# Optimization experiments

Measured on AMD Instinct MI355X. Metric: run time of the kernel, lower is better.

Reference implementation:

```python
import jax, jax.numpy as jnp
import numpy as np

N, E, Z, H = 16384, 131072, 128, 8
ZH = Z // H
CUTOFF = 5.0


def _dense(key, din, dout, bias=True):
    kw, kb = jax.random.split(key)
    W = (jax.random.normal(kw, (din, dout), jnp.float32) / np.sqrt(din)).astype(jnp.float32)
    if bias:
        return W, jnp.zeros((dout,), jnp.float32)
    return W


def setup_inputs() -> dict:
    key = jax.random.key(0)
    ks = jax.random.split(key, 24)
    edge_index = jax.random.randint(ks[0], (2, E), 0, N)
    h_N_1_Z = jax.random.normal(ks[1], (N, 1, Z), jnp.float32)
    mu_N_L2_Z = jax.random.normal(ks[2], (N, 3, Z), jnp.float32) * 0.1
    ev = jax.random.normal(ks[3], (E, 3), jnp.float32)
    edge_vec_E_3 = ev / jnp.linalg.norm(ev, axis=-1, keepdims=True)
    edge_emb_E_Z = jax.random.normal(ks[4], (E, Z), jnp.float32)
    edge_weight_E = jax.random.uniform(ks[5], (E,), jnp.float32, 0.5, CUTOFF)
    deg = jax.ops.segment_sum(jnp.ones((E,), jnp.float32), edge_index[1], num_segments=N)
    num_edges_expanded_E = deg[edge_index[1]]
    inp = dict(edge_index=edge_index, h_N_1_Z=h_N_1_Z, mu_N_L2_Z=mu_N_L2_Z,
               edge_vec_E_3=edge_vec_E_3, edge_emb_E_Z=edge_emb_E_Z,
               edge_weight_E=edge_weight_E, num_edges_expanded_E=num_edges_expanded_E)
    inp['W_q'], inp['b_q'] = _dense(ks[6], Z, Z)
    inp['W_k'], inp['b_k'] = _dense(ks[7], Z, Z)
    inp['W_gs1'], inp['b_gs1'] = _dense(ks[8], Z, Z)
    inp['W_gs2'], inp['b_gs2'] = _dense(ks[9], Z, 3 * Z)
    inp['W_gv1'], inp['b_gv1'] = _dense(ks[10], Z, Z)
    inp['W_gv2'], inp['b_gv2'] = _dense(ks[11], Z, 3 * Z)
    inp['W_phik'], inp['b_phik'] = _dense(ks[12], Z, Z)
    inp['W_re'], inp['b_re'] = _dense(ks[13], Z, 3 * Z)
    inp['W_vq'] = _dense(ks[14], Z, Z, bias=False)   # vecq_w, no bias
    inp['W_vk0'] = _dense(ks[15], Z, Z, bias=False)  # veck_w[0] (lmax=1), no bias
    inp['W_lin'], inp['b_lin'] = _dense(ks[16], Z, Z)  # lin_w_linear
    inp['W_eu1'], inp['b_eu1'] = _dense(ks[17], Z, Z)  # edge_attr_up MLP [Z,Z,Z]
    inp['W_eu2'], inp['b_eu2'] = _dense(ks[18], Z, Z)
    return inp


def reference(edge_index, h_N_1_Z, mu_N_L2_Z, edge_vec_E_3, edge_emb_E_Z,
              edge_weight_E, num_edges_expanded_E,
              W_q, b_q, W_k, b_k, W_gs1, b_gs1, W_gs2, b_gs2,
              W_gv1, b_gv1, W_gv2, b_gv2, W_phik, b_phik, W_re, b_re,
              W_vq, W_vk0, W_lin, b_lin, W_eu1, b_eu1, W_eu2, b_eu2):
    silu = jax.nn.silu
    src, dst = edge_index[0], edge_index[1]  # messages j->i aggregated at dst=i
    hs = h_N_1_Z[:, 0]                        # (N, Z); layernorm='' -> identity
    q = (hs @ W_q + b_q).reshape(N, H, ZH)
    k = (hs @ W_k + b_k).reshape(N, H, ZH)
    x3 = silu(hs @ W_gs1 + b_gs1) @ W_gs2 + b_gs2    # gamma_s: (N, 3Z)
    val3 = silu(hs @ W_gv1 + b_gv1) @ W_gv2 + b_gv2  # gamma_v: (N, 3Z)
    r_attn = silu(edge_emb_E_Z @ W_phik + b_phik).reshape(E, H, ZH)
    r_ij = edge_emb_E_Z @ W_re + b_re                # (E, 3Z)

    # per-edge multi-head attention with segment softmax over target node
    logits = jnp.sum(q[dst] * k[src] * r_attn, axis=-1)        # (E, H)
    m = jax.ops.segment_max(logits, dst, num_segments=N)
    ex = jnp.exp(logits - m[dst])
    den = jax.ops.segment_sum(ex, dst, num_segments=N)
    attn = ex / den[dst]
    attn = attn * (jnp.sqrt(num_edges_expanded_E)[:, None] / np.float32(np.sqrt(Z)))

    sea = (attn[..., None] * val3[src].reshape(E, H, 3 * ZH)).reshape(E, 3 * Z)
    cut = 0.5 * (jnp.cos(jnp.pi * edge_weight_E / CUTOFF) + 1.0) * (edge_weight_E < CUTOFF)
    x_ij = cut[:, None] * sea * (x3[src] * r_ij)               # (E, 3Z)
    o_s, o_d, o_t = x_ij[:, :Z], x_ij[:, Z:2 * Z], x_ij[:, 2 * Z:]
    dmu_ij = o_d[:, None, :] * edge_vec_E_3[..., None] + o_t[:, None, :] * mu_N_L2_Z[src]  # (E,3,Z)

    h_out = h_N_1_Z + jax.ops.segment_sum(o_s, dst, num_segments=N)[:, None, :]
    mu_out = mu_N_L2_Z + jax.ops.segment_sum(dmu_ij, dst, num_segments=N)

    # edge update (sep_vecj, lmax=1 -> single degree block)
    w1 = jnp.einsum('nlz,ze->nle', mu_out, W_vq)
    w2 = jnp.einsum('nlz,ze->nle', mu_out, W_vk0)
    w1_d = jnp.sum(w1[dst] * edge_vec_E_3[..., None], axis=1)  # (E, evec)
    w2_d = jnp.sum(w2[src] * edge_vec_E_3[..., None], axis=1)
    w_dot = jnp.tanh((w1_d * w2_d) @ W_lin + b_lin)            # gated='gatedt'
    f_up = silu(edge_emb_E_Z @ W_eu1 + b_eu1) @ W_eu2 + b_eu2  # edge_attr_up MLP
    df_ij = edge_emb_E_Z + f_up * w_dot
    return h_out, mu_out, df_ij
```

## Files before the change

### kernel.cpp

```cpp
#include <hip/hip_runtime.h>
#include <math.h>

#define NN 16384
#define EE 131072
#define ZZ 128
#define HH 8

typedef short bf16x8 __attribute__((ext_vector_type(8)));
typedef float f32x4 __attribute__((ext_vector_type(4)));
typedef unsigned short ushort4v __attribute__((ext_vector_type(4)));
typedef unsigned short ushort8v __attribute__((ext_vector_type(8)));

__device__ __forceinline__ float silu_f(float x) { return x / (1.0f + __expf(-x)); }

__device__ __forceinline__ unsigned short f2bf(float x) {
    unsigned u = __float_as_uint(x);
    unsigned r = (u >> 16) & 1u;
    u += 0x7fffu + r;
    return (unsigned short)(u >> 16);
}
__device__ __forceinline__ float bf2f(unsigned short x) {
    return __uint_as_float(((unsigned)x) << 16);
}

__device__ __forceinline__ f32x4 mfma16(bf16x8 a, bf16x8 b, f32x4 c) {
    return __builtin_amdgcn_mfma_f32_16x16x32_bf16(a, b, c, 0, 0, 0);
}

__device__ __forceinline__ unsigned fenc(float x) {
    unsigned b = __float_as_uint(x);
    return (b & 0x80000000u) ? ~b : (b | 0x80000000u);
}
__device__ __forceinline__ float fdec(unsigned e) {
    unsigned b = (e & 0x80000000u) ? (e & 0x7FFFFFFFu) : ~e;
    return __uint_as_float(b);
}

__device__ __forceinline__ void stageB(const unsigned short* Wt, char* lB, int t) {
    const uint4* Wg = (const uint4*)Wt;
#pragma unroll
    for (int i = 0; i < 8; ++i) {
        const int cid = t + i * 256;
        const int n = cid >> 4, c16 = cid & 15;
        *(uint4*)(lB + ((n * 256 + c16 * 16) ^ ((n & 7) << 4))) = Wg[cid];
    }
}

struct WPrep {
    const float* w[13];
    int P[13];
    int tile0[14];
};

__global__ __launch_bounds__(128) void prep_weights(WPrep wp, unsigned short* wt) {
    int b = blockIdx.x, wi = 0;
    while (b >= wp.tile0[wi + 1]) ++wi;
    const int cg = (b - wp.tile0[wi]) * 128;
    const float* w = wp.w[wi];
    unsigned short* o = wt + (size_t)wp.tile0[wi] * 16384;
    const int P = wp.P[wi];
    const int t = threadIdx.x;
    for (int k0 = 0; k0 < 128; k0 += 8) {
        ushort8v v;
#pragma unroll
        for (int j = 0; j < 8; ++j) v[j] = f2bf(w[(size_t)(k0 + j) * P + cg + t]);
        *(ushort8v*)(o + (size_t)(cg + t) * 128 + k0) = v;
    }
}

struct BPrep {
    const float* b[13];
    int off[14];
};

__global__ __launch_bounds__(256) void prep_bias(BPrep bp, float* bcat) {
    const int idx = blockIdx.x * 256 + threadIdx.x;
    if (idx >= 2432) return;
    int wi = 0;
    while (idx >= bp.off[wi + 1]) ++wi;
    bcat[idx] = bp.b[wi] ? bp.b[wi][idx - bp.off[wi]] : 0.f;
}

template <int ACT, int INBF, int DUMP>
__global__ __launch_bounds__(256, 2) void mm_bf16(
    const void* __restrict__ Av, const unsigned short* __restrict__ Wt,
    const float* __restrict__ bias, unsigned short* __restrict__ C,
    const unsigned short* __restrict__ aux, unsigned short* __restrict__ dumpA,
    int P, int As)
{
    __shared__ uint4 lA4[2048];
    __shared__ uint4 lB4[2048];
    char* lA = (char*)lA4;
    char* lB = (char*)lB4;
    const int t = threadIdx.x;
    const size_t row0 = (size_t)blockIdx.x * 128;
    const int cg = blockIdx.y * 128;
    if (INBF) {
        const uint4* Ag = (const uint4*)((const unsigned short*)Av + row0 * As);
        const int rs = As >> 3;
#pragma unroll
        for (int i = 0; i < 8; ++i) {
            const int chunk = t + i * 256;
            const int r = chunk >> 4, c16 = chunk & 15;
            *(uint4*)(lA + ((r * 256 + c16 * 16) ^ ((r & 7) << 4))) = Ag[r * rs + c16];
        }
    } else {
        const float4* Ag = (const float4*)((const float*)Av + row0 * As);
        const int rs = As >> 2;
#pragma unroll
        for (int i = 0; i < 16; ++i) {
            const int f4 = t + i * 256;
            const int r = f4 >> 5, c4 = f4 & 31;
            const float4 v = Ag[r * rs + c4];
            ushort4v bb;
            bb.x = f2bf(v.x); bb.y = f2bf(v.y); bb.z = f2bf(v.z); bb.w = f2bf(v.w);
            *(ushort4v*)(lA + ((r * 256 + c4 * 8) ^ ((r & 7) << 4))) = bb;
        }
    }
    stageB(Wt + (size_t)cg * 128, lB, t);
    __syncthreads();
    if (DUMP) {
#pragma unroll
        for (int i = 0; i < 8; ++i) {
            const int ch = t + i * 256;
            const int row = ch >> 4, cpos = ch & 15;
            const uint4 v = *(const uint4*)(lA + ((row * 256 + cpos * 16) ^ ((row & 7) << 4)));
            *(uint4*)(dumpA + (row0 + row) * 128 + cpos * 8) = v;
        }
    }
    const int lane = t & 63, wid = t >> 6;
    const int rbase = (wid >> 1) * 64, cbase = (wid & 1) * 64;
    const int lr = lane & 15, lgp = lane >> 4;
    f32x4 acc[4][4];
#pragma unroll
    for (int i = 0; i < 4; ++i)
#pragma unroll
        for (int j = 0; j < 4; ++j) acc[i][j] = (f32x4){0.f, 0.f, 0.f, 0.f};
#pragma unroll
    for (int ks = 0; ks < 4; ++ks) {
        bf16x8 av[4], bv[4];
#pragma unroll
        for (int mt = 0; mt < 4; ++mt) {
            const int r = rbase + mt * 16 + lr;
            av[mt] = *(const bf16x8*)(lA + ((r * 256 + ks * 64 + lgp * 16) ^ ((r & 7) << 4)));
        }
#pragma unroll
        for (int nt = 0; nt < 4; ++nt) {
            const int c = cbase + nt * 16 + lr;
            bv[nt] = *(const bf16x8*)(lB + ((c * 256 + ks * 64 + lgp * 16) ^ ((c & 7) << 4)));
        }
#pragma unroll
        for (int mt = 0; mt < 4; ++mt)
#pragma unroll
            for (int nt = 0; nt < 4; ++nt)
                acc[mt][nt] = mfma16(av[mt], bv[nt], acc[mt][nt]);
    }
    __syncthreads();
#pragma unroll
    for (int nt = 0; nt < 4; ++nt) {
        const int col = cbase + nt * 16 + lr;
        const int gcol = cg + col;
        const float b = bias[gcol];
#pragma unroll
        for (int mt = 0; mt < 4; ++mt) {
#pragma unroll
            for (int j = 0; j < 4; ++j) {
                const int row = rbase + mt * 16 + lgp * 4 + j;
                float v = acc[mt][nt][j] + b;
                if (ACT == 1) v = silu_f(v);
                if (ACT == 2) v = v * bf2f(aux[(row0 + row) * (size_t)P + gcol]);
                *(unsigned short*)(lB + ((row * 256 + col * 2) ^ ((row & 7) << 4))) = f2bf(v);
            }
        }
    }
    __syncthreads();
#pragma unroll
    for (int i = 0; i < 8; ++i) {
        const int ch = t + i * 256;
        const int row = ch >> 4, cpos = ch & 15;
        const uint4 v = *(const uint4*)(lB + ((row * 256 + cpos * 16) ^ ((row & 7) << 4)));
        *(uint4*)(C + (row0 + row) * (size_t)P + cg + cpos * 8) = v;
    }
}

__global__ __launch_bounds__(256, 2) void combine_mfma(
    const unsigned short* __restrict__ embb, const unsigned short* __restrict__ Wt_re,
    const float* __restrict__ bre, const float* __restrict__ lg,
    const float* __restrict__ den, const float* __restrict__ nee,
    const int* __restrict__ dst, const float* __restrict__ ew,
    unsigned short* __restrict__ osb, unsigned short* __restrict__ odb,
    unsigned short* __restrict__ otb)
{
    __shared__ uint4 lA4[2048];
    __shared__ uint4 lB4[2048];
    __shared__ float attnS[128 * 8];
    __shared__ float cutS[128];
    char* lA = (char*)lA4;
    char* lB = (char*)lB4;
    const int t = threadIdx.x;
    const size_t e0 = (size_t)blockIdx.x * 128;
    {
        const uint4* Ag = (const uint4*)(embb + e0 * 128);
#pragma unroll
        for (int i = 0; i < 8; ++i) {
            const int chunk = t + i * 256;
            const int r = chunk >> 4, c16 = chunk & 15;
            *(uint4*)(lA + ((r * 256 + c16 * 16) ^ ((r & 7) << 4))) = Ag[chunk];
        }
    }
    stageB(Wt_re, lB, t);
    {
        const int er = t >> 1;
        const size_t e = e0 + er;
        const int h0 = (t & 1) * 4;
        const int d = dst[e];
        const float sc = sqrtf(nee[e]) * 0.08838834764831845f;
        const float4 ex4 = *(const float4*)(lg + e * 8 + h0);
        const float4 dn4 = *(const float4*)(den + (size_t)d * 8 + h0);
        float4 a4;
        a4.x = ex4.x / dn4.x * sc; a4.y = ex4.y / dn4.y * sc;
        a4.z = ex4.z / dn4.z * sc; a4.w = ex4.w / dn4.w * sc;
        *(float4*)(attnS + er * 8 + h0) = a4;
        if ((t & 1) == 0) {
            const float w = ew[e];
            cutS[er] = (w < 5.0f) ? 0.5f * (cosf(w * 0.62831853071795864f) + 1.0f) : 0.0f;
        }
    }
    __syncthreads();
    const int lane = t & 63, wid = t >> 6;
    const int rbase = (wid >> 1) * 64, cbase = (wid & 1) * 64;
    const int lr = lane & 15, lgp = lane >> 4;
    bf16x8 avh[4][4];
#pragma unroll
    for (int ks = 0; ks < 4; ++ks)
#pragma unroll
        for (int mt = 0; mt < 4; ++mt) {
            const int r = rbase + mt * 16 + lr;
            avh[ks][mt] = *(const bf16x8*)(lA + ((r * 256 + ks * 64 + lgp * 16) ^ ((r & 7) << 4)));
        }
    __syncthreads();
    unsigned short* bufs[3] = {osb, odb, otb};
    for (int cg3 = 0; cg3 < 3; ++cg3) {
        f32x4 acc[4][4];
#pragma unroll
        for (int i = 0; i < 4; ++i)
#pragma unroll
            for (int j = 0; j < 4; ++j) acc[i][j] = (f32x4){0.f, 0.f, 0.f, 0.f};
#pragma unroll
        for (int ks = 0; ks < 4; ++ks) {
            bf16x8 bv[4];
#pragma unroll
            for (int nt = 0; nt < 4; ++nt) {
                const int c = cbase + nt * 16 + lr;
                bv[nt] = *(const bf16x8*)(lB + ((c * 256 + ks * 64 + lgp * 16) ^ ((c & 7) << 4)));
            }
#pragma unroll
            for (int mt = 0; mt < 4; ++mt)
#pragma unroll
                for (int nt = 0; nt < 4; ++nt)
                    acc[mt][nt] = mfma16(avh[ks][mt], bv[nt], acc[mt][nt]);
        }
        const int cgo = cg3 * 128;
#pragma unroll
        for (int nt = 0; nt < 4; ++nt) {
            const int col = cbase + nt * 16 + lr;
            const int gcol = cgo + col;
            const int head = gcol / 48;
            const float b = bre[gcol];
#pragma unroll
            for (int mt = 0; mt < 4; ++mt) {
#pragma unroll
                for (int j = 0; j < 4; ++j) {
                    const int row = rbase + mt * 16 + lgp * 4 + j;
                    const float o = (acc[mt][nt][j] + b) * attnS[row * 8 + head] * cutS[row];
                    *(unsigned short*)(lA + ((row * 256 + col * 2) ^ ((row & 7) << 4))) = f2bf(o);
                }
            }
        }
        __syncthreads();
        unsigned short* buf = bufs[cg3];
#pragma unroll
        for (int i = 0; i < 8; ++i) {
            const int ch = t + i * 256;
            const int row = ch >> 4, cpos = ch & 15;
            const uint4 v = *(const uint4*)(lA + ((row * 256 + cpos * 16) ^ ((row & 7) << 4)));
            *(uint4*)(buf + (e0 + row) * 128 + cpos * 8) = v;
        }
        if (cg3 < 2) stageB(Wt_re + (size_t)(cg3 + 1) * 16384, lB, t);
        __syncthreads();
    }
}

__global__ __launch_bounds__(256, 2) void wdot_fused(
    const unsigned short* __restrict__ w12, const float* __restrict__ ev,
    const int* __restrict__ src, const int* __restrict__ dst,
    const unsigned short* __restrict__ Wt_lin, const float* __restrict__ bl,
    const unsigned short* __restrict__ embb, const unsigned short* __restrict__ fup,
    float* __restrict__ df)
{
    __shared__ uint4 lA4[2048];
    __shared__ uint4 lB4[2048];
    char* lA = (char*)lA4;
    char* lB = (char*)lB4;
    const int t = threadIdx.x;
    const size_t e0 = (size_t)blockIdx.x * 128;
    stageB(Wt_lin, lB, t);
#pragma unroll
    for (int i = 0; i < 8; ++i) {
        const int chunk = t + i * 256;
        const int r = chunk >> 4, c8 = chunk & 15;
        const size_t e = e0 + r;
        const int s = src[e], d = dst[e];
        const float e0v = ev[e * 3 + 0], e1v = ev[e * 3 + 1], e2v = ev[e * 3 + 2];
        const ushort8v a0 = *(const ushort8v*)(w12 + ((size_t)d * 3 + 0) * 256 + c8 * 8);
        const ushort8v a1 = *(const ushort8v*)(w12 + ((size_t)d * 3 + 1) * 256 + c8 * 8);
        const ushort8v a2 = *(const ushort8v*)(w12 + ((size_t)d * 3 + 2) * 256 + c8 * 8);
        const ushort8v c0 = *(const ushort8v*)(w12 + ((size_t)s * 3 + 0) * 256 + 128 + c8 * 8);
        const ushort8v c1 = *(const ushort8v*)(w12 + ((size_t)s * 3 + 1) * 256 + 128 + c8 * 8);
        const ushort8v c2 = *(const ushort8v*)(w12 + ((size_t)s * 3 + 2) * 256 + 128 + c8 * 8);
        ushort8v o;
#pragma unroll
        for (int j = 0; j < 8; ++j) {
            const float av = e0v * bf2f(a0[j]) + e1v * bf2f(a1[j]) + e2v * bf2f(a2[j]);
            const float bv = e0v * bf2f(c0[j]) + e1v * bf2f(c1[j]) + e2v * bf2f(c2[j]);
            o[j] = f2bf(av * bv);
        }
        *(ushort8v*)(lA + ((r * 256 + c8 * 16) ^ ((r & 7) << 4))) = o;
    }
    __syncthreads();
    const int lane = t & 63, wid = t >> 6;
    const int rbase = (wid >> 1) * 64, cbase = (wid & 1) * 64;
    const int lr = lane & 15, lgp = lane >> 4;
    f32x4 acc[4][4];
#pragma unroll
    for (int i = 0; i < 4; ++i)
#pragma unroll
        for (int j = 0; j < 4; ++j) acc[i][j] = (f32x4){0.f, 0.f, 0.f, 0.f};
#pragma unroll
    for (int ks = 0; ks < 4; ++ks) {
        bf16x8 av[4], bv[4];
#pragma unroll
        for (int mt = 0; mt < 4; ++mt) {
            const int r = rbase + mt * 16 + lr;
            av[mt] = *(const bf16x8*)(lA + ((r * 256 + ks * 64 + lgp * 16) ^ ((r & 7) << 4)));
        }
#pragma unroll
        for (int nt = 0; nt < 4; ++nt) {
            const int c = cbase + nt * 16 + lr;
            bv[nt] = *(const bf16x8*)(lB + ((c * 256 + ks * 64 + lgp * 16) ^ ((c & 7) << 4)));
        }
#pragma unroll
        for (int mt = 0; mt < 4; ++mt)
#pragma unroll
            for (int nt = 0; nt < 4; ++nt)
                acc[mt][nt] = mfma16(av[mt], bv[nt], acc[mt][nt]);
    }
#pragma unroll
    for (int nt = 0; nt < 4; ++nt) {
        const int col = cbase + nt * 16 + lr;
        const float b = bl[col];
#pragma unroll
        for (int mt = 0; mt < 4; ++mt) {
#pragma unroll
            for (int j = 0; j < 4; ++j) {
                const size_t base = (e0 + rbase + mt * 16 + lgp * 4 + j) * 128 + col;
                const float v = tanhf(acc[mt][nt][j] + b);
                df[base] = bf2f(embb[base]) + bf2f(fup[base]) * v;
            }
        }
    }
}

__global__ __launch_bounds__(256) void logits_max_kernel(
    const unsigned short* __restrict__ qkb, const unsigned short* __restrict__ ra,
    const int* __restrict__ src, const int* __restrict__ dst,
    float* __restrict__ lg, unsigned* __restrict__ mEnc)
{
    const int idx = blockIdx.x * 256 + threadIdx.x;
    const int e = idx >> 3, h = idx & 7;
    const int s = src[e], d = dst[e];
    const ushort8v* qp = (const ushort8v*)(qkb + (size_t)d * 256 + h * 16);
    const ushort8v* kp = (const ushort8v*)(qkb + (size_t)s * 256 + 128 + h * 16);
    const ushort8v* rp = (const ushort8v*)(ra + (size_t)e * 128 + h * 16);
    float sum = 0.f;
#pragma unroll
    for (int i = 0; i < 2; ++i) {
        const ushort8v a = qp[i], b = kp[i], r = rp[i];
#pragma unroll
        for (int j = 0; j < 8; ++j) sum += bf2f(a[j]) * bf2f(b[j]) * bf2f(r[j]);
    }
    lg[idx] = sum;
    atomicMax(&mEnc[d * 8 + h], fenc(sum));
}

__global__ __launch_bounds__(256) void exp_den_kernel(
    const int* __restrict__ dst, const unsigned* __restrict__ mEnc,
    float* __restrict__ lg, float* __restrict__ den)
{
    const int idx = blockIdx.x * 256 + threadIdx.x;
    const int e = idx >> 3, h = idx & 7;
    const int d = dst[e];
    const float m = fdec(mEnc[d * 8 + h]);
    const float ex = __expf(lg[idx] - m);
    lg[idx] = ex;
    atomicAdd(&den[d * 8 + h], ex);
}

__global__ __launch_bounds__(256) void hist_kernel(const int* __restrict__ dst, int* __restrict__ counts) {
    const int e = blockIdx.x * 256 + threadIdx.x;
    atomicAdd(&counts[dst[e]], 1);
}

__global__ __launch_bounds__(256) void scan_kernel(const int* __restrict__ counts,
                                                   int* __restrict__ row_start,
                                                   int* __restrict__ cursor) {
    __shared__ int part[256];
    const int t = threadIdx.x;
    const int base = t * 64;
    int local[64];
    int s = 0;
#pragma unroll
    for (int i = 0; i < 64; ++i) { local[i] = s; s += counts[base + i]; }
    part[t] = s;
    __syncthreads();
    for (int off = 1; off < 256; off <<= 1) {
        int v = (t >= off) ? part[t - off] : 0;
        __syncthreads();
        part[t] += v;
        __syncthreads();
    }
    const int prev = (t == 0) ? 0 : part[t - 1];
#pragma unroll
    for (int i = 0; i < 64; ++i) {
        const int v = prev + local[i];
        row_start[base + i] = v;
        cursor[base + i] = v;
    }
    if (t == 255) row_start[NN] = prev + s;
}

__global__ __launch_bounds__(256) void fill_kernel(const int* __restrict__ dst,
                                                   int* __restrict__ cursor,
                                                   int* __restrict__ perm) {
    const int e = blockIdx.x * 256 + threadIdx.x;
    const int p = atomicAdd(&cursor[dst[e]], 1);
    perm[p] = e;
}

__global__ __launch_bounds__(128) void gather_kernel(
    const int* __restrict__ row_start, const int* __restrict__ perm,
    const int* __restrict__ src, const unsigned short* __restrict__ osb,
    const unsigned short* __restrict__ odb, const unsigned short* __restrict__ otb,
    const unsigned short* __restrict__ xv, const float* __restrict__ ev,
    const float* __restrict__ h_in, const float* __restrict__ mu_in,
    float* __restrict__ h_out, float* __restrict__ mu_out)
{
    const int n = blockIdx.x;
    const int t = threadIdx.x;
    const int beg = row_start[n], end = row_start[n + 1];
    float hacc = h_in[(size_t)n * 128 + t];
    float m0 = mu_in[(size_t)n * 384 + t];
    float m1 = mu_in[(size_t)n * 384 + 128 + t];
    float m2 = mu_in[(size_t)n * 384 + 256 + t];
    for (int i = beg; i < end; ++i) {
        const int e = perm[i];
        const int s = src[e];
        const float e0 = ev[e * 3 + 0], e1 = ev[e * 3 + 1], e2 = ev[e * 3 + 2];
        const unsigned short* xp = xv + (size_t)s * 384 + t;
        const float osv = bf2f(osb[(size_t)e * 128 + t]) * bf2f(xp[0]);
        const float odv = bf2f(odb[(size_t)e * 128 + t]) * bf2f(xp[128]);
        const float otv = bf2f(otb[(size_t)e * 128 + t]) * bf2f(xp[256]);
        const float* msp = mu_in + (size_t)s * 384 + t;
        hacc += osv;
        m0 += odv * e0 + otv * msp[0];
        m1 += odv * e1 + otv * msp[128];
        m2 += odv * e2 + otv * msp[256];
    }
    h_out[(size_t)n * 128 + t] = hacc;
    mu_out[(size_t)n * 384 + t] = m0;
    mu_out[(size_t)n * 384 + 128 + t] = m1;
    mu_out[(size_t)n * 384 + 256 + t] = m2;
}

extern "C" void kernel_launch(void* const* d_in, const int* in_sizes, int n_in,
                              void* d_out, int out_size, void* d_ws, size_t ws_size,
                              hipStream_t stream) {
    const int* eidx = (const int*)d_in[0];
    const int* src = eidx;
    const int* dst = eidx + EE;
    const float* h_in  = (const float*)d_in[1];
    const float* mu_in = (const float*)d_in[2];
    const float* ev    = (const float*)d_in[3];
    const float* emb   = (const float*)d_in[4];
    const float* ewt   = (const float*)d_in[5];
    const float* nee   = (const float*)d_in[6];
    const float* W_q   = (const float*)d_in[7];  const float* b_q   = (const float*)d_in[8];
    const float* W_k   = (const float*)d_in[9];  const float* b_k   = (const float*)d_in[10];
    const float* W_gs1 = (const float*)d_in[11]; const float* b_gs1 = (const float*)d_in[12];
    const float* W_gs2 = (const float*)d_in[13]; const float* b_gs2 = (const float*)d_in[14];
    const float* W_gv1 = (const float*)d_in[15]; const float* b_gv1 = (const float*)d_in[16];
    const float* W_gv2 = (const float*)d_in[17]; const float* b_gv2 = (const float*)d_in[18];
    const float* W_phik= (const float*)d_in[19]; const float* b_phik= (const float*)d_in[20];
    const float* W_re  = (const float*)d_in[21]; const float* b_re  = (const float*)d_in[22];
    const float* W_vq  = (const float*)d_in[23];
    const float* W_vk0 = (const float*)d_in[24];
    const float* W_lin = (const float*)d_in[25]; const float* b_lin = (const float*)d_in[26];
    const float* W_eu1 = (const float*)d_in[27]; const float* b_eu1 = (const float*)d_in[28];
    const float* W_eu2 = (const float*)d_in[29]; const float* b_eu2 = (const float*)d_in[30];

    float* out    = (float*)d_out;
    float* h_out  = out;
    float* mu_out = out + (size_t)NN * ZZ;
    float* df     = out + (size_t)NN * ZZ * 4;

    const size_t NZ = (size_t)NN * ZZ, N3Z = (size_t)NN * 3 * ZZ, EZ = (size_t)EE * ZZ;
    const size_t EH = (size_t)EE * HH, NHs = (size_t)NN * HH;
    char* p = (char*)d_ws;
    unsigned short* qkb   = (unsigned short*)p; p += NZ * 2 * 2;
    unsigned short* tmpn2 = (unsigned short*)p; p += NZ * 2 * 2;
    unsigned short* x3b   = (unsigned short*)p; p += N3Z * 2;
    unsigned short* xv    = (unsigned short*)p; p += N3Z * 2;
    unsigned short* w12   = (unsigned short*)p; p += N3Z * 2 * 2;
    unsigned short* embb  = (unsigned short*)p; p += EZ * 2;
    unsigned short* rab   = (unsigned short*)p; p += EZ * 2;
    unsigned short* tmpe  = (unsigned short*)p; p += EZ * 2;
    unsigned short* fup   = (unsigned short*)p; p += EZ * 2;
    unsigned short* osb   = (unsigned short*)p; p += EZ * 2;
    unsigned short* odb   = (unsigned short*)p; p += EZ * 2;
    unsigned short* otb   = (unsigned short*)p; p += EZ * 2;
    float* lg             = (float*)p;          p += EH * 4;
    unsigned short* wt    = (unsigned short*)p; p += 2432 * 128 * 2;
    float* bcat           = (float*)p;          p += 2432 * 4;
    unsigned* mEnc        = (unsigned*)p;       p += NHs * 4;
    float* den            = (float*)p;          p += NHs * 4;
    int* counts           = (int*)p;            p += NN * 4;
    int* cursor           = (int*)p;            p += NN * 4;
    int* row_start        = (int*)p;            p += (NN + 1) * 4;
    int* perm             = (int*)p;            p += EE * 4;

    const float* wsrc[13] = {W_q, W_k, W_gs1, W_gv1, W_gs2, W_gv2, W_phik,
                             W_re, W_vq, W_vk0, W_lin, W_eu1, W_eu2};
    const float* bsrc[13] = {b_q, b_k, b_gs1, b_gv1, b_gs2, b_gv2, b_phik,
                             b_re, nullptr, nullptr, b_lin, b_eu1, b_eu2};
    const int Ps[13] = {128, 128, 128, 128, 384, 384, 128, 384, 128, 128, 128, 128, 128};
    WPrep wp; BPrep bp;
    int tiles = 0;
    for (int i = 0; i < 13; ++i) {
        wp.w[i] = wsrc[i]; wp.P[i] = Ps[i]; wp.tile0[i] = tiles;
        bp.b[i] = bsrc[i]; bp.off[i] = tiles * 128;
        tiles += Ps[i] / 128;
    }
    wp.tile0[13] = tiles; bp.off[13] = tiles * 128;
    unsigned short* wT[13]; const float* bC[13];
    for (int i = 0; i < 13; ++i) { wT[i] = wt + (size_t)wp.tile0[i] * 16384; bC[i] = bcat + bp.off[i]; }

    dim3 blk(256);
    prep_weights<<<dim3(tiles), dim3(128), 0, stream>>>(wp, wt);
    prep_bias<<<dim3(10), blk, 0, stream>>>(bp, bcat);
    mm_bf16<0,0,0><<<dim3(NN/128, 2), blk, 0, stream>>>(h_in, wT[0], bC[0], qkb, nullptr, nullptr, 256, 128);
    mm_bf16<1,0,0><<<dim3(NN/128, 2), blk, 0, stream>>>(h_in, wT[2], bC[2], tmpn2, nullptr, nullptr, 256, 128);
    mm_bf16<0,1,0><<<dim3(NN/128, 3), blk, 0, stream>>>(tmpn2, wT[4], bC[4], x3b, nullptr, nullptr, 384, 256);
    mm_bf16<2,1,0><<<dim3(NN/128, 3), blk, 0, stream>>>(tmpn2 + 128, wT[5], bC[5], xv, x3b, nullptr, 384, 256);
    mm_bf16<1,0,1><<<dim3(EE/128, 1), blk, 0, stream>>>(emb, wT[11], bC[11], tmpe, nullptr, embb, 128, 128);
    mm_bf16<0,1,0><<<dim3(EE/128, 1), blk, 0, stream>>>(tmpe, wT[12], bC[12], fup, nullptr, nullptr, 128, 128);
    mm_bf16<1,1,0><<<dim3(EE/128, 1), blk, 0, stream>>>(embb, wT[6], bC[6], rab, nullptr, nullptr, 128, 128);
    hipMemsetAsync(counts, 0, NN * 4, stream);
    hipMemsetAsync(mEnc, 0, NHs * 4, stream);
    hipMemsetAsync(den, 0, NHs * 4, stream);
    hist_kernel<<<dim3(EE/256), blk, 0, stream>>>(dst, counts);
    scan_kernel<<<dim3(1), blk, 0, stream>>>(counts, row_start, cursor);
    fill_kernel<<<dim3(EE/256), blk, 0, stream>>>(dst, cursor, perm);
    logits_max_kernel<<<dim3(EH/256), blk, 0, stream>>>(qkb, rab, src, dst, lg, mEnc);
    exp_den_kernel<<<dim3(EH/256), blk, 0, stream>>>(dst, mEnc, lg, den);
    combine_mfma<<<dim3(EE/128), blk, 0, stream>>>(
        embb, wT[7], bC[7], lg, den, nee, dst, ewt, osb, odb, otb);
    gather_kernel<<<dim3(NN), dim3(128), 0, stream>>>(
        row_start, perm, src, osb, odb, otb, xv, ev, h_in, mu_in, h_out, mu_out);
    mm_bf16<0,0,0><<<dim3(3*NN/128, 2), blk, 0, stream>>>(mu_out, wT[8], bC[8], w12, nullptr, nullptr, 256, 128);
    wdot_fused<<<dim3(EE/128), blk, 0, stream>>>(
        w12, ev, src, dst, wT[10], bC[10], embb, fup, df);
}
```

Baseline: 460.4 us.

## Fuse segment softmax into CSR attention kernel and drop LDS weight staging

```diff
diff --git a/kernel.cpp b/kernel.cpp
--- a/kernel.cpp
+++ b/kernel.cpp
@@ -25,15 +25,6 @@
 
 __device__ __forceinline__ f32x4 mfma16(bf16x8 a, bf16x8 b, f32x4 c) {
     return __builtin_amdgcn_mfma_f32_16x16x32_bf16(a, b, c, 0, 0, 0);
-}
-
-__device__ __forceinline__ unsigned fenc(float x) {
-    unsigned b = __float_as_uint(x);
-    return (b & 0x80000000u) ? ~b : (b | 0x80000000u);
-}
-__device__ __forceinline__ float fdec(unsigned e) {
-    unsigned b = (e & 0x80000000u) ? (e & 0x7FFFFFFFu) : ~e;
-    return __uint_as_float(b);
 }
 
 __device__ __forceinline__ void stageB(const unsigned short* Wt, char* lB, int t) {
@@ -183,20 +174,71 @@
     }
 }
 
-__global__ __launch_bounds__(256, 2) void combine_mfma(
+__global__ __launch_bounds__(256) void attn_kernel(
+    const int* __restrict__ row_start, const int* __restrict__ perm,
+    const int* __restrict__ src, const unsigned short* __restrict__ qkb,
+    const unsigned short* __restrict__ rab, const float* __restrict__ ewt,
+    float* __restrict__ attnw)
+{
+    const int t = threadIdx.x;
+    const int n = blockIdx.x * 4 + (t >> 6);
+    const int lane = t & 63;
+    const int el = lane >> 3, h = lane & 7;
+    const int beg = row_start[n], end = row_start[n + 1];
+    if (beg == end) return;
+    const ushort8v q0 = *(const ushort8v*)(qkb + (size_t)n * 256 + h * 16);
+    const ushort8v q1 = *(const ushort8v*)(qkb + (size_t)n * 256 + h * 16 + 8);
+    float m = -1e30f, den = 0.f;
+    for (int i0 = beg; i0 < end; i0 += 8) {
+        const int i = i0 + el;
+        const bool valid = i < end;
+        const int e = perm[valid ? i : beg];
+        const int s = src[e];
+        const ushort8v k0 = *(const ushort8v*)(qkb + (size_t)s * 256 + 128 + h * 16);
+        const ushort8v k1 = *(const ushort8v*)(qkb + (size_t)s * 256 + 128 + h * 16 + 8);
+        const ushort8v r0 = *(const ushort8v*)(rab + (size_t)e * 128 + h * 16);
+        const ushort8v r1 = *(const ushort8v*)(rab + (size_t)e * 128 + h * 16 + 8);
+        float lgv = 0.f;
+#pragma unroll
+        for (int j = 0; j < 8; ++j) lgv += bf2f(q0[j]) * bf2f(k0[j]) * bf2f(r0[j]);
+#pragma unroll
+        for (int j = 0; j < 8; ++j) lgv += bf2f(q1[j]) * bf2f(k1[j]) * bf2f(r1[j]);
+        if (!valid) lgv = -1e30f;
+        else attnw[(size_t)e * 8 + h] = lgv;
+        float cm = lgv;
+        cm = fmaxf(cm, __shfl_xor(cm, 8));
+        cm = fmaxf(cm, __shfl_xor(cm, 16));
+        cm = fmaxf(cm, __shfl_xor(cm, 32));
+        const float nm = fmaxf(m, cm);
+        float ex = valid ? __expf(lgv - nm) : 0.f;
+        float cd = ex;
+        cd += __shfl_xor(cd, 8);
+        cd += __shfl_xor(cd, 16);
+        cd += __shfl_xor(cd, 32);
+        den = den * __expf(m - nm) + cd;
+        m = nm;
+    }
+    const float sc = sqrtf((float)(end - beg)) * 0.08838834764831845f / den;
+    for (int i0 = beg; i0 < end; i0 += 8) {
+        const int i = i0 + el;
+        if (i >= end) continue;
+        const int e = perm[i];
+        const float w = ewt[e];
+        const float cut = (w < 5.0f) ? 0.5f * (cosf(w * 0.62831853071795864f) + 1.0f) : 0.0f;
+        const float lgv = attnw[(size_t)e * 8 + h];
+        attnw[(size_t)e * 8 + h] = __expf(lgv - m) * sc * cut;
+    }
+}
+
+__global__ __launch_bounds__(256, 4) void combine_mfma(
     const unsigned short* __restrict__ embb, const unsigned short* __restrict__ Wt_re,
-    const float* __restrict__ bre, const float* __restrict__ lg,
-    const float* __restrict__ den, const float* __restrict__ nee,
-    const int* __restrict__ dst, const float* __restrict__ ew,
+    const float* __restrict__ bre, const float* __restrict__ attnw,
     unsigned short* __restrict__ osb, unsigned short* __restrict__ odb,
     unsigned short* __restrict__ otb)
 {
     __shared__ uint4 lA4[2048];
-    __shared__ uint4 lB4[2048];
     __shared__ float attnS[128 * 8];
-    __shared__ float cutS[128];
     char* lA = (char*)lA4;
-    char* lB = (char*)lB4;
     const int t = threadIdx.x;
     const size_t e0 = (size_t)blockIdx.x * 128;
     {
@@ -208,39 +250,14 @@
             *(uint4*)(lA + ((r * 256 + c16 * 16) ^ ((r & 7) << 4))) = Ag[chunk];
         }
     }
-    stageB(Wt_re, lB, t);
-    {
-        const int er = t >> 1;
-        const size_t e = e0 + er;
-        const int h0 = (t & 1) * 4;
-        const int d = dst[e];
-        const float sc = sqrtf(nee[e]) * 0.08838834764831845f;
-        const float4 ex4 = *(const float4*)(lg + e * 8 + h0);
-        const float4 dn4 = *(const float4*)(den + (size_t)d * 8 + h0);
-        float4 a4;
-        a4.x = ex4.x / dn4.x * sc; a4.y = ex4.y / dn4.y * sc;
-        a4.z = ex4.z / dn4.z * sc; a4.w = ex4.w / dn4.w * sc;
-        *(float4*)(attnS + er * 8 + h0) = a4;
-        if ((t & 1) == 0) {
-            const float w = ew[e];
-            cutS[er] = (w < 5.0f) ? 0.5f * (cosf(w * 0.62831853071795864f) + 1.0f) : 0.0f;
-        }
-    }
+    ((float4*)attnS)[t] = ((const float4*)(attnw + e0 * 8))[t];
     __syncthreads();
     const int lane = t & 63, wid = t >> 6;
     const int rbase = (wid >> 1) * 64, cbase = (wid & 1) * 64;
     const int lr = lane & 15, lgp = lane >> 4;
-    bf16x8 avh[4][4];
-#pragma unroll
-    for (int ks = 0; ks < 4; ++ks)
-#pragma unroll
-        for (int mt = 0; mt < 4; ++mt) {
-            const int r = rbase + mt * 16 + lr;
-            avh[ks][mt] = *(const bf16x8*)(lA + ((r * 256 + ks * 64 + lgp * 16) ^ ((r & 7) << 4)));
-        }
-    __syncthreads();
     unsigned short* bufs[3] = {osb, odb, otb};
     for (int cg3 = 0; cg3 < 3; ++cg3) {
+        const unsigned short* Wp = Wt_re + (size_t)cg3 * 16384;
         f32x4 acc[4][4];
 #pragma unroll
         for (int i = 0; i < 4; ++i)
@@ -248,50 +265,45 @@
             for (int j = 0; j < 4; ++j) acc[i][j] = (f32x4){0.f, 0.f, 0.f, 0.f};
 #pragma unroll
         for (int ks = 0; ks < 4; ++ks) {
-            bf16x8 bv[4];
+            bf16x8 av[4], bv[4];
+#pragma unroll
+            for (int mt = 0; mt < 4; ++mt) {
+                const int r = rbase + mt * 16 + lr;
+                av[mt] = *(const bf16x8*)(lA + ((r * 256 + ks * 64 + lgp * 16) ^ ((r & 7) << 4)));
+            }
+#pragma unroll
+            for (int nt = 0; nt < 4; ++nt)
+                bv[nt] = *(const bf16x8*)(Wp + (size_t)(cbase + nt * 16 + lr) * 128 + ks * 32 + lgp * 8);
+#pragma unroll
+            for (int mt = 0; mt < 4; ++mt)
+#pragma unroll
+                for (int nt = 0; nt < 4; ++nt)
+                    acc[mt][nt] = mfma16(bv[nt], av[mt], acc[mt][nt]);
+        }
+        unsigned short* buf = bufs[cg3];
+        const int cgo = cg3 * 128;
+#pragma unroll
+        for (int mt = 0; mt < 4; ++mt) {
+            const int row = rbase + mt * 16 + lr;
+            const float* aS = attnS + row * 8;
 #pragma unroll
             for (int nt = 0; nt < 4; ++nt) {
-                const int c = cbase + nt * 16 + lr;
-                bv[nt] = *(const bf16x8*)(lB + ((c * 256 + ks * 64 + lgp * 16) ^ ((c & 7) << 4)));
+                const int col0 = cbase + nt * 16 + lgp * 4;
+                const int gcol = cgo + col0;
+                const float coef = aS[gcol / 48];
+                const float4 b4 = *(const float4*)(bre + gcol);
+                ushort4v st;
+                st.x = f2bf((acc[mt][nt][0] + b4.x) * coef);
+                st.y = f2bf((acc[mt][nt][1] + b4.y) * coef);
+                st.z = f2bf((acc[mt][nt][2] + b4.z) * coef);
+                st.w = f2bf((acc[mt][nt][3] + b4.w) * coef);
+                *(ushort4v*)(buf + (e0 + row) * 128 + col0) = st;
             }
-#pragma unroll
-            for (int mt = 0; mt < 4; ++mt)
-#pragma unroll
-                for (int nt = 0; nt < 4; ++nt)
-                    acc[mt][nt] = mfma16(avh[ks][mt], bv[nt], acc[mt][nt]);
-        }
-        const int cgo = cg3 * 128;
-#pragma unroll
-        for (int nt = 0; nt < 4; ++nt) {
-            const int col = cbase + nt * 16 + lr;
-            const int gcol = cgo + col;
-            const int head = gcol / 48;
-            const float b = bre[gcol];
-#pragma unroll
-            for (int mt = 0; mt < 4; ++mt) {
-#pragma unroll
-                for (int j = 0; j < 4; ++j) {
-                    const int row = rbase + mt * 16 + lgp * 4 + j;
-                    const float o = (acc[mt][nt][j] + b) * attnS[row * 8 + head] * cutS[row];
-                    *(unsigned short*)(lA + ((row * 256 + col * 2) ^ ((row & 7) << 4))) = f2bf(o);
-                }
-            }
-        }
-        __syncthreads();
-        unsigned short* buf = bufs[cg3];
-#pragma unroll
-        for (int i = 0; i < 8; ++i) {
-            const int ch = t + i * 256;
-            const int row = ch >> 4, cpos = ch & 15;
-            const uint4 v = *(const uint4*)(lA + ((row * 256 + cpos * 16) ^ ((row & 7) << 4)));
-            *(uint4*)(buf + (e0 + row) * 128 + cpos * 8) = v;
-        }
-        if (cg3 < 2) stageB(Wt_re + (size_t)(cg3 + 1) * 16384, lB, t);
-        __syncthreads();
-    }
-}
-
-__global__ __launch_bounds__(256, 2) void wdot_fused(
+        }
+    }
+}
+
+__global__ __launch_bounds__(256, 3) void wdot_fused(
     const unsigned short* __restrict__ w12, const float* __restrict__ ev,
     const int* __restrict__ src, const int* __restrict__ dst,
     const unsigned short* __restrict__ Wt_lin, const float* __restrict__ bl,
@@ -299,12 +311,9 @@
     float* __restrict__ df)
 {
     __shared__ uint4 lA4[2048];
-    __shared__ uint4 lB4[2048];
     char* lA = (char*)lA4;
-    char* lB = (char*)lB4;
     const int t = threadIdx.x;
     const size_t e0 = (size_t)blockIdx.x * 128;
-    stageB(Wt_lin, lB, t);
 #pragma unroll
     for (int i = 0; i < 8; ++i) {
         const int chunk = t + i * 256;
@@ -345,65 +354,32 @@
             av[mt] = *(const bf16x8*)(lA + ((r * 256 + ks * 64 + lgp * 16) ^ ((r & 7) << 4)));
         }
 #pragma unroll
+        for (int nt = 0; nt < 4; ++nt)
+            bv[nt] = *(const bf16x8*)(Wt_lin + (size_t)(cbase + nt * 16 + lr) * 128 + ks * 32 + lgp * 8);
+#pragma unroll
+        for (int mt = 0; mt < 4; ++mt)
+#pragma unroll
+            for (int nt = 0; nt < 4; ++nt)
+                acc[mt][nt] = mfma16(bv[nt], av[mt], acc[mt][nt]);
+    }
+#pragma unroll
+    for (int mt = 0; mt < 4; ++mt) {
+        const int row = rbase + mt * 16 + lr;
+#pragma unroll
         for (int nt = 0; nt < 4; ++nt) {
-            const int c = cbase + nt * 16 + lr;
-            bv[nt] = *(const bf16x8*)(lB + ((c * 256 + ks * 64 + lgp * 16) ^ ((c & 7) << 4)));
-        }
-#pragma unroll
-        for (int mt = 0; mt < 4; ++mt)
-#pragma unroll
-            for (int nt = 0; nt < 4; ++nt)
-                acc[mt][nt] = mfma16(av[mt], bv[nt], acc[mt][nt]);
-    }
-#pragma unroll
-    for (int nt = 0; nt < 4; ++nt) {
-        const int col = cbase + nt * 16 + lr;
-        const float b = bl[col];
-#pragma unroll
-        for (int mt = 0; mt < 4; ++mt) {
-#pragma unroll
-            for (int j = 0; j < 4; ++j) {
-                const size_t base = (e0 + rbase + mt * 16 + lgp * 4 + j) * 128 + col;
-                const float v = tanhf(acc[mt][nt][j] + b);
-                df[base] = bf2f(embb[base]) + bf2f(fup[base]) * v;
-            }
-        }
-    }
-}
-
-__global__ __launch_bounds__(256) void logits_max_kernel(
-    const unsigned short* __restrict__ qkb, const unsigned short* __restrict__ ra,
-    const int* __restrict__ src, const int* __restrict__ dst,
-    float* __restrict__ lg, unsigned* __restrict__ mEnc)
-{
-    const int idx = blockIdx.x * 256 + threadIdx.x;
-    const int e = idx >> 3, h = idx & 7;
-    const int s = src[e], d = dst[e];
-    const ushort8v* qp = (const ushort8v*)(qkb + (size_t)d * 256 + h * 16);
-    const ushort8v* kp = (const ushort8v*)(qkb + (size_t)s * 256 + 128 + h * 16);
-    const ushort8v* rp = (const ushort8v*)(ra + (size_t)e * 128 + h * 16);
-    float sum = 0.f;
-#pragma unroll
-    for (int i = 0; i < 2; ++i) {
-        const ushort8v a = qp[i], b = kp[i], r = rp[i];
-#pragma unroll
-        for (int j = 0; j < 8; ++j) sum += bf2f(a[j]) * bf2f(b[j]) * bf2f(r[j]);
-    }
-    lg[idx] = sum;
-    atomicMax(&mEnc[d * 8 + h], fenc(sum));
-}
-
-__global__ __launch_bounds__(256) void exp_den_kernel(
-    const int* __restrict__ dst, const unsigned* __restrict__ mEnc,
-    float* __restrict__ lg, float* __restrict__ den)
-{
-    const int idx = blockIdx.x * 256 + threadIdx.x;
-    const int e = idx >> 3, h = idx & 7;
-    const int d = dst[e];
-    const float m = fdec(mEnc[d * 8 + h]);
-    const float ex = __expf(lg[idx] - m);
-    lg[idx] = ex;
-    atomicAdd(&den[d * 8 + h], ex);
+            const int col0 = cbase + nt * 16 + lgp * 4;
+            const float4 b4 = *(const float4*)(bl + col0);
+            const size_t base = (e0 + row) * 128 + col0;
+            const ushort4v em = *(const ushort4v*)(embb + base);
+            const ushort4v fu = *(const ushort4v*)(fup + base);
+            float4 o;
+            o.x = bf2f(em.x) + bf2f(fu.x) * tanhf(acc[mt][nt][0] + b4.x);
+            o.y = bf2f(em.y) + bf2f(fu.y) * tanhf(acc[mt][nt][1] + b4.y);
+            o.z = bf2f(em.z) + bf2f(fu.z) * tanhf(acc[mt][nt][2] + b4.z);
+            o.w = bf2f(em.w) + bf2f(fu.w) * tanhf(acc[mt][nt][3] + b4.w);
+            *(float4*)(df + base) = o;
+        }
+    }
 }
 
 __global__ __launch_bounds__(256) void hist_kernel(const int* __restrict__ dst, int* __restrict__ counts) {
@@ -447,7 +423,7 @@
     perm[p] = e;
 }
 
-__global__ __launch_bounds__(128) void gather_kernel(
+__global__ __launch_bounds__(256) void gather_kernel(
     const int* __restrict__ row_start, const int* __restrict__ perm,
     const int* __restrict__ src, const unsigned short* __restrict__ osb,
     const unsigned short* __restrict__ odb, const unsigned short* __restrict__ otb,
@@ -455,8 +431,8 @@
     const float* __restrict__ h_in, const float* __restrict__ mu_in,
     float* __restrict__ h_out, float* __restrict__ mu_out)
 {
-    const int n = blockIdx.x;
-    const int t = threadIdx.x;
+    const int n = blockIdx.x * 2 + (threadIdx.x >> 7);
+    const int t = threadIdx.x & 127;
     const int beg = row_start[n], end = row_start[n + 1];
     float hacc = h_in[(size_t)n * 128 + t];
     float m0 = mu_in[(size_t)n * 384 + t];
@@ -493,7 +469,6 @@
     const float* ev    = (const float*)d_in[3];
     const float* emb   = (const float*)d_in[4];
     const float* ewt   = (const float*)d_in[5];
-    const float* nee   = (const float*)d_in[6];
     const float* W_q   = (const float*)d_in[7];  const float* b_q   = (const float*)d_in[8];
     const float* W_k   = (const float*)d_in[9];  const float* b_k   = (const float*)d_in[10];
     const float* W_gs1 = (const float*)d_in[11]; const float* b_gs1 = (const float*)d_in[12];
@@ -514,7 +489,7 @@
     float* df     = out + (size_t)NN * ZZ * 4;
 
     const size_t NZ = (size_t)NN * ZZ, N3Z = (size_t)NN * 3 * ZZ, EZ = (size_t)EE * ZZ;
-    const size_t EH = (size_t)EE * HH, NHs = (size_t)NN * HH;
+    const size_t EH = (size_t)EE * HH;
     char* p = (char*)d_ws;
     unsigned short* qkb   = (unsigned short*)p; p += NZ * 2 * 2;
     unsigned short* tmpn2 = (unsigned short*)p; p += NZ * 2 * 2;
@@ -528,11 +503,9 @@
     unsigned short* osb   = (unsigned short*)p; p += EZ * 2;
     unsigned short* odb   = (unsigned short*)p; p += EZ * 2;
     unsigned short* otb   = (unsigned short*)p; p += EZ * 2;
-    float* lg             = (float*)p;          p += EH * 4;
+    float* attnw          = (float*)p;          p += EH * 4;
     unsigned short* wt    = (unsigned short*)p; p += 2432 * 128 * 2;
     float* bcat           = (float*)p;          p += 2432 * 4;
-    unsigned* mEnc        = (unsigned*)p;       p += NHs * 4;
-    float* den            = (float*)p;          p += NHs * 4;
     int* counts           = (int*)p;            p += NN * 4;
     int* cursor           = (int*)p;            p += NN * 4;
     int* row_start        = (int*)p;            p += (NN + 1) * 4;
@@ -565,16 +538,13 @@
     mm_bf16<0,1,0><<<dim3(EE/128, 1), blk, 0, stream>>>(tmpe, wT[12], bC[12], fup, nullptr, nullptr, 128, 128);
     mm_bf16<1,1,0><<<dim3(EE/128, 1), blk, 0, stream>>>(embb, wT[6], bC[6], rab, nullptr, nullptr, 128, 128);
     hipMemsetAsync(counts, 0, NN * 4, stream);
-    hipMemsetAsync(mEnc, 0, NHs * 4, stream);
-    hipMemsetAsync(den, 0, NHs * 4, stream);
     hist_kernel<<<dim3(EE/256), blk, 0, stream>>>(dst, counts);
     scan_kernel<<<dim3(1), blk, 0, stream>>>(counts, row_start, cursor);
     fill_kernel<<<dim3(EE/256), blk, 0, stream>>>(dst, cursor, perm);
-    logits_max_kernel<<<dim3(EH/256), blk, 0, stream>>>(qkb, rab, src, dst, lg, mEnc);
-    exp_den_kernel<<<dim3(EH/256), blk, 0, stream>>>(dst, mEnc, lg, den);
+    attn_kernel<<<dim3(NN/4), blk, 0, stream>>>(row_start, perm, src, qkb, rab, ewt, attnw);
     combine_mfma<<<dim3(EE/128), blk, 0, stream>>>(
-        embb, wT[7], bC[7], lg, den, nee, dst, ewt, osb, odb, otb);
-    gather_kernel<<<dim3(NN), dim3(128), 0, stream>>>(
+        embb, wT[7], bC[7], attnw, osb, odb, otb);
+    gather_kernel<<<dim3(NN/2), blk, 0, stream>>>(
         row_start, perm, src, osb, odb, otb, xv, ev, h_in, mu_in, h_out, mu_out);
     mm_bf16<0,0,0><<<dim3(3*NN/128, 2), blk, 0, stream>>>(mu_out, wT[8], bC[8], w12, nullptr, nullptr, 256, 128);
     wdot_fused<<<dim3(EE/128), blk, 0, stream>>>(
```

After: 416.4 us. 1.11x faster.
